# Kernel tuning notes

Measured on AMD Instinct MI355X. Metric: run time of the kernel, lower is better.

## Reference

```python
import jax, jax.numpy as jnp
import numpy as np

B, N, T, E, H, R = 8, 64, 128, 128, 8, 4
DH = E // H


def setup_inputs() -> dict:
    key = jax.random.key(0)
    ks = jax.random.split(key, 14)
    s = 1.0 / np.sqrt(E)
    return {
        "node_memory": jax.random.normal(ks[0], (B, N, T, E), jnp.float32),
        "subgraph_memory": jax.random.normal(ks[1], (B, N, T, E, R - 1), jnp.float32),
        "Wq": jax.random.normal(ks[2], (E, E), jnp.float32) * s,
        "bq": jnp.zeros((E,), jnp.float32),
        "Wk": jax.random.normal(ks[3], (E, E), jnp.float32) * s,
        "bk": jnp.zeros((E,), jnp.float32),
        "Wv": jax.random.normal(ks[4], (E, E), jnp.float32) * s,
        "bv": jnp.zeros((E,), jnp.float32),
        "in_w": jax.random.normal(ks[5], (3 * E, E), jnp.float32) * s,
        "in_b": jnp.zeros((3 * E,), jnp.float32),
        "out_w": jax.random.normal(ks[6], (E, E), jnp.float32) * s,
        "out_b": jnp.zeros((E,), jnp.float32),
        "fc_w": jax.random.normal(ks[7], (E, R * E), jnp.float32) * (1.0 / np.sqrt(R * E)),
        "fc_b": jnp.zeros((E,), jnp.float32),
    }


def reference(node_memory, subgraph_memory, Wq, bq, Wk, bk, Wv, bv,
              in_w, in_b, out_w, out_b, fc_w, fc_b):
    # combined: [B,N,T,R,E] = concat(node[...,None,:], subgraph permuted)
    combined = jnp.concatenate(
        [node_memory[..., None, :], jnp.swapaxes(subgraph_memory, -1, -2)], axis=-2)
    # outer QKV projections
    Q = jnp.einsum("bntrf,ef->bntre", combined, Wq) + bq
    K = jnp.einsum("bntrf,ef->bntre", combined, Wk) + bk
    V = jnp.einsum("bntrf,ef->bntre", combined, Wv) + bv
    # nn.MultiheadAttention in-projection
    q = jnp.einsum("bntre,fe->bntrf", Q, in_w[:E]) + in_b[:E]
    k = jnp.einsum("bntre,fe->bntrf", K, in_w[E:2 * E]) + in_b[E:2 * E]
    v = jnp.einsum("bntre,fe->bntrf", V, in_w[2 * E:]) + in_b[2 * E:]
    # split heads: [B,N,T,R,H,DH]
    q = q.reshape(B, N, T, R, H, DH) * (1.0 / np.sqrt(DH))
    k = k.reshape(B, N, T, R, H, DH)
    v = v.reshape(B, N, T, R, H, DH)
    scores = jnp.einsum("bntrhd,bntshd->bnthrs", q, k)  # [B,N,T,H,R,R]
    attn = jax.nn.softmax(scores, axis=-1)
    o = jnp.einsum("bnthrs,bntshd->bntrhd", attn, v).reshape(B, N, T, R, E)
    o = jnp.einsum("bntre,fe->bntrf", o, out_w) + out_b
    # concat the R representations and fuse
    o = o.reshape(B, N, T, R * E)
    return jnp.einsum("bntc,ec->bnte", o, fc_w) + fc_b
```

## Files before the change

kernel.cpp:

```cpp
#include <hip/hip_runtime.h>
#include <hip/hip_bf16.h>

constexpr int cE  = 128;
constexpr int cR  = 4;
constexpr int cNT = 65536;

typedef short s8v  __attribute__((ext_vector_type(8)));
typedef float f4v  __attribute__((ext_vector_type(4)));

static __device__ __forceinline__ unsigned short f2bf(float x) {
    union { float f; unsigned int u; } v; v.f = x;
    unsigned int r = v.u + 0x7fffu + ((v.u >> 16) & 1u);
    return (unsigned short)(r >> 16);
}

#define QB(x, C) __int_as_float(__builtin_amdgcn_update_dpp( \
            0, __float_as_int(x), C, 0xF, 0xF, false))

__global__ __launch_bounds__(256) void k_prep(
    const float* __restrict__ Wq, const float* __restrict__ Wk, const float* __restrict__ Wv,
    const float* __restrict__ in_w, const float* __restrict__ out_w, const float* __restrict__ fc_w,
    const float* __restrict__ bq, const float* __restrict__ bk, const float* __restrict__ bv,
    const float* __restrict__ in_b, const float* __restrict__ out_b, const float* __restrict__ fc_b,
    unsigned short* __restrict__ wqkv, unsigned short* __restrict__ meff,
    float* __restrict__ bqkv, float* __restrict__ beff)
{
    int bid = blockIdx.x;
    if (bid < 1792) {
        int gt = bid * 256 + (int)threadIdx.x;
        int o  = gt >> 2;
        int p  = gt & 3;
        float s;
        if (o < 3 * cE * cE) {
            int w   = o >> 14;
            int rem = o & (cE * cE - 1);
            int f = rem >> 7, g = rem & 127;
            const float* Wsel = (w == 0) ? Wq : ((w == 1) ? Wk : Wv);
            const float* iw = in_w + (size_t)(w * cE + f) * cE + p * 32;
            const float* wp = Wsel + (size_t)(p * 32) * cE + g;
            float s0 = 0.f, s1 = 0.f;
            #pragma unroll
            for (int e = 0; e < 32; e += 2) {
                s0 += iw[e]     * wp[(size_t)e * cE];
                s1 += iw[e + 1] * wp[(size_t)(e + 1) * cE];
            }
            s = s0 + s1;
            s += __shfl_xor(s, 1);
            s += __shfl_xor(s, 2);
            if (w == 0) s *= 0.25f;
            if (p == 0) wqkv[o] = f2bf(s);
        } else {
            int i2 = o - 3 * cE * cE;
            int e1 = i2 >> 9;
            int c  = i2 & 511;
            const float* fw = fc_w + (size_t)e1 * 512 + (c >> 7) * cE + p * 32;
            int ee = c & 127;
            const float* ow = out_w + (size_t)(p * 32) * cE + ee;
            float s0 = 0.f, s1 = 0.f;
            #pragma unroll
            for (int ff = 0; ff < 32; ff += 2) {
                s0 += fw[ff]     * ow[(size_t)ff * cE];
                s1 += fw[ff + 1] * ow[(size_t)(ff + 1) * cE];
            }
            s = s0 + s1;
            s += __shfl_xor(s, 1);
            s += __shfl_xor(s, 2);
            if (p == 0) meff[i2] = f2bf(s);
        }
    } else {
        int idx = (bid - 1792) * 256 + (int)threadIdx.x;
        if (idx < 384) {
            int w = idx >> 7, f = idx & 127;
            const float* bsel = (w == 0) ? bq : ((w == 1) ? bk : bv);
            const float* iw = in_w + (size_t)(w * cE + f) * cE;
            float s = 0.f;
            for (int e = 0; e < cE; ++e) s += iw[e] * bsel[e];
            s += in_b[w * cE + f];
            if (w == 0) s *= 0.25f;
            bqkv[idx] = s;
        } else {
            int f = idx - 384;
            float s = 0.f;
            for (int c = 0; c < 512; ++c) s += fc_w[(size_t)f * 512 + c] * out_b[c & 127];
            beff[f] = s + fc_b[f];
        }
    }
}

#define TOKB   64
#define TOKC   16
#define PITCH  136
#define OPITCH 520

__global__ __launch_bounds__(512) void k_main(
    const float* __restrict__ node, const float* __restrict__ sub,
    const unsigned short* __restrict__ wqkv,
    const unsigned short* __restrict__ meff,
    const float* __restrict__ bqkv,
    const float* __restrict__ beff,
    float* __restrict__ out)
{
    __shared__ unsigned short sA[64 * PITCH];
    __shared__ unsigned short sO[16 * OPITCH];

    const int tid  = threadIdx.x;
    const int lane = tid & 63;
    const int wv   = tid >> 6;
    const int l15  = lane & 15;
    const int lq   = lane >> 4;

    const int tokBlock = blockIdx.x * TOKB;
    const int stok = tid >> 5;
    const int seg  = tid & 31;
    const int e0   = seg * 4;

    #pragma clang loop unroll(disable)
    for (int chunk = 0; chunk < TOKB / TOKC; ++chunk) {
        const int tokBase = tokBlock + chunk * TOKC;
        __syncthreads();

        {
            const float* np = node + (size_t)(tokBase + stok) * cE + e0;
            const float* sp = sub  + (size_t)(tokBase + stok) * 384 + seg * 12;
            float4 vn = *(const float4*)np;
            float4 f0 = *(const float4*)(sp + 0);
            float4 f1 = *(const float4*)(sp + 4);
            float4 f2 = *(const float4*)(sp + 8);
            *(ushort4*)&sA[(stok * cR) * PITCH + e0] =
                make_ushort4(f2bf(vn.x), f2bf(vn.y), f2bf(vn.z), f2bf(vn.w));
            *(ushort4*)&sA[(stok * cR + 1) * PITCH + e0] =
                make_ushort4(f2bf(f0.x), f2bf(f0.w), f2bf(f1.z), f2bf(f2.y));
            *(ushort4*)&sA[(stok * cR + 2) * PITCH + e0] =
                make_ushort4(f2bf(f0.y), f2bf(f1.x), f2bf(f1.w), f2bf(f2.z));
            *(ushort4*)&sA[(stok * cR + 3) * PITCH + e0] =
                make_ushort4(f2bf(f0.z), f2bf(f1.y), f2bf(f2.x), f2bf(f2.w));
        }
        __syncthreads();

        f4v qa[4], ka[4], va[4];
        #pragma unroll
        for (int rt = 0; rt < 4; ++rt) {
            qa[rt] = (f4v){0.f, 0.f, 0.f, 0.f};
            ka[rt] = (f4v){0.f, 0.f, 0.f, 0.f};
            va[rt] = (f4v){0.f, 0.f, 0.f, 0.f};
        }
        #pragma unroll
        for (int kc = 0; kc < 4; ++kc) {
            const int koff = kc * 32 + lq * 8;
            s8v a0 = *(const s8v*)&sA[(0 * 16 + l15) * PITCH + koff];
            s8v a1 = *(const s8v*)&sA[(1 * 16 + l15) * PITCH + koff];
            s8v a2 = *(const s8v*)&sA[(2 * 16 + l15) * PITCH + koff];
            s8v a3 = *(const s8v*)&sA[(3 * 16 + l15) * PITCH + koff];
            const size_t fo = (size_t)(wv * 16 + l15) * cE + koff;
            s8v wq_ = *(const s8v*)(wqkv + fo);
            s8v wk_ = *(const s8v*)(wqkv + 16384 + fo);
            s8v wv_ = *(const s8v*)(wqkv + 32768 + fo);
            qa[0] = __builtin_amdgcn_mfma_f32_16x16x32_bf16(wq_, a0, qa[0], 0, 0, 0);
            qa[1] = __builtin_amdgcn_mfma_f32_16x16x32_bf16(wq_, a1, qa[1], 0, 0, 0);
            qa[2] = __builtin_amdgcn_mfma_f32_16x16x32_bf16(wq_, a2, qa[2], 0, 0, 0);
            qa[3] = __builtin_amdgcn_mfma_f32_16x16x32_bf16(wq_, a3, qa[3], 0, 0, 0);
            ka[0] = __builtin_amdgcn_mfma_f32_16x16x32_bf16(wk_, a0, ka[0], 0, 0, 0);
            ka[1] = __builtin_amdgcn_mfma_f32_16x16x32_bf16(wk_, a1, ka[1], 0, 0, 0);
            ka[2] = __builtin_amdgcn_mfma_f32_16x16x32_bf16(wk_, a2, ka[2], 0, 0, 0);
            ka[3] = __builtin_amdgcn_mfma_f32_16x16x32_bf16(wk_, a3, ka[3], 0, 0, 0);
            va[0] = __builtin_amdgcn_mfma_f32_16x16x32_bf16(wv_, a0, va[0], 0, 0, 0);
            va[1] = __builtin_amdgcn_mfma_f32_16x16x32_bf16(wv_, a1, va[1], 0, 0, 0);
            va[2] = __builtin_amdgcn_mfma_f32_16x16x32_bf16(wv_, a2, va[2], 0, 0, 0);
            va[3] = __builtin_amdgcn_mfma_f32_16x16x32_bf16(wv_, a3, va[3], 0, 0, 0);
        }
        {
            const int fb = wv * 16 + lq * 4;
            float4 b0 = *(const float4*)(bqkv + fb);
            float4 b1 = *(const float4*)(bqkv + cE + fb);
            float4 b2 = *(const float4*)(bqkv + 2 * cE + fb);
            #pragma unroll
            for (int rt = 0; rt < 4; ++rt) {
                qa[rt][0] += b0.x; qa[rt][1] += b0.y;
                qa[rt][2] += b0.z; qa[rt][3] += b0.w;
                ka[rt][0] += b1.x; ka[rt][1] += b1.y;
                ka[rt][2] += b1.z; ka[rt][3] += b1.w;
                va[rt][0] += b2.x; va[rt][1] += b2.y;
                va[rt][2] += b2.z; va[rt][3] += b2.w;
            }
        }

        {
            const int r  = l15 & 3;
            const int tq = l15 >> 2;
            #pragma unroll
            for (int rt = 0; rt < 4; ++rt) {
                f4v q = qa[rt], k = ka[rt], v = va[rt];
                float s0 = QB(k[0],0x00)*q[0] + QB(k[1],0x00)*q[1]
                         + QB(k[2],0x00)*q[2] + QB(k[3],0x00)*q[3];
                float s1 = QB(k[0],0x55)*q[0] + QB(k[1],0x55)*q[1]
                         + QB(k[2],0x55)*q[2] + QB(k[3],0x55)*q[3];
                float s2 = QB(k[0],0xAA)*q[0] + QB(k[1],0xAA)*q[1]
                         + QB(k[2],0xAA)*q[2] + QB(k[3],0xAA)*q[3];
                float s3 = QB(k[0],0xFF)*q[0] + QB(k[1],0xFF)*q[1]
                         + QB(k[2],0xFF)*q[2] + QB(k[3],0xFF)*q[3];
                s0 += __shfl_xor(s0, 16); s0 += __shfl_xor(s0, 32);
                s1 += __shfl_xor(s1, 16); s1 += __shfl_xor(s1, 32);
                s2 += __shfl_xor(s2, 16); s2 += __shfl_xor(s2, 32);
                s3 += __shfl_xor(s3, 16); s3 += __shfl_xor(s3, 32);
                float m = fmaxf(fmaxf(s0, s1), fmaxf(s2, s3));
                float p0 = __expf(s0 - m), p1 = __expf(s1 - m);
                float p2 = __expf(s2 - m), p3 = __expf(s3 - m);
                float inv = 1.f / (p0 + p1 + p2 + p3);
                p0 *= inv; p1 *= inv; p2 *= inv; p3 *= inv;
                float o0 = p0*QB(v[0],0x00) + p1*QB(v[0],0x55)
                         + p2*QB(v[0],0xAA) + p3*QB(v[0],0xFF);
                float o1 = p0*QB(v[1],0x00) + p1*QB(v[1],0x55)
                         + p2*QB(v[1],0xAA) + p3*QB(v[1],0xFF);
                float o2 = p0*QB(v[2],0x00) + p1*QB(v[2],0x55)
                         + p2*QB(v[2],0xAA) + p3*QB(v[2],0xFF);
                float o3 = p0*QB(v[3],0x00) + p1*QB(v[3],0x55)
                         + p2*QB(v[3],0xAA) + p3*QB(v[3],0xFF);
                int tok = rt * 4 + tq;
                *(ushort4*)&sO[tok * OPITCH + r * cE + wv * 16 + lq * 4] =
                    make_ushort4(f2bf(o0), f2bf(o1), f2bf(o2), f2bf(o3));
            }
        }
        __syncthreads();

        {
            f4v acc = (f4v){0.f, 0.f, 0.f, 0.f};
            #pragma unroll 4
            for (int kc = 0; kc < 16; ++kc) {
                int koff = kc * 32 + lq * 8;
                s8v a = *(const s8v*)&sO[l15 * OPITCH + koff];
                s8v b = *(const s8v*)(meff + (size_t)(wv * 16 + l15) * 512 + koff);
                acc = __builtin_amdgcn_mfma_f32_16x16x32_bf16(b, a, acc, 0, 0, 0);
            }
            const int col = wv * 16 + lq * 4;
            float4 b4 = *(const float4*)&beff[col];
            *(float4*)&out[(size_t)(tokBase + l15) * cE + col] =
                make_float4(acc[0] + b4.x, acc[1] + b4.y,
                            acc[2] + b4.z, acc[3] + b4.w);
        }
    }
}

extern "C" void kernel_launch(void* const* d_in, const int* in_sizes, int n_in,
                              void* d_out, int out_size, void* d_ws, size_t ws_size,
                              hipStream_t stream) {
    const float* node  = (const float*)d_in[0];
    const float* sub   = (const float*)d_in[1];
    const float* Wq    = (const float*)d_in[2];
    const float* bq    = (const float*)d_in[3];
    const float* Wk    = (const float*)d_in[4];
    const float* bk    = (const float*)d_in[5];
    const float* Wv    = (const float*)d_in[6];
    const float* bv    = (const float*)d_in[7];
    const float* in_w  = (const float*)d_in[8];
    const float* in_b  = (const float*)d_in[9];
    const float* out_w = (const float*)d_in[10];
    const float* out_b = (const float*)d_in[11];
    const float* fc_w  = (const float*)d_in[12];
    const float* fc_b  = (const float*)d_in[13];

    unsigned short* ws_wqkv = (unsigned short*)d_ws;
    unsigned short* ws_meff = ws_wqkv + 3 * cE * cE;
    float* ws_bqkv = (float*)((char*)d_ws + (size_t)(3 * cE * cE + cE * cR * cE) * 2);
    float* ws_beff = ws_bqkv + 3 * cE;

    k_prep<<<dim3(1794), dim3(256), 0, stream>>>(Wq, Wk, Wv, in_w, out_w, fc_w,
                                                 bq, bk, bv, in_b, out_b, fc_b,
                                                 ws_wqkv, ws_meff, ws_bqkv, ws_beff);
    k_main<<<dim3(cNT / TOKB), dim3(512), 0, stream>>>(node, sub, ws_wqkv, ws_meff,
                                                       ws_bqkv, ws_beff, (float*)d_out);
}
```

Baseline: 327.5 us.

## Split fused attention kernel into attention stage and separate output GEMM

Splits the fused per-chunk kernel into two kernels. The first computes QKV projections and the small attention per 16-token block, writing a bf16 concatenated output to workspace. The second runs the fused out/fc projection as a tiled GEMM over 64-token blocks with LDS staging. This aims to raise parallelism and improve reuse in the final GEMM, at the cost of an extra global round-trip of the intermediate. The old fused kernel is kept as a fallback when the workspace is too small.

```diff
diff --git a/kernel.cpp b/kernel.cpp
--- a/kernel.cpp
+++ b/kernel.cpp
@@ -87,12 +87,198 @@
     }
 }
 
-#define TOKB   64
 #define TOKC   16
 #define PITCH  136
 #define OPITCH 520
 
-__global__ __launch_bounds__(512) void k_main(
+__global__ __launch_bounds__(512) void k_mainA(
+    const float* __restrict__ node, const float* __restrict__ sub,
+    const unsigned short* __restrict__ wqkv,
+    const float* __restrict__ bqkv,
+    unsigned short* __restrict__ oconcat)
+{
+    __shared__ unsigned short sA[64 * PITCH];
+
+    const int tid  = threadIdx.x;
+    const int lane = tid & 63;
+    const int wv   = tid >> 6;
+    const int l15  = lane & 15;
+    const int lq   = lane >> 4;
+
+    const int tokBase = blockIdx.x * TOKC;
+    const int stok = tid >> 5;
+    const int seg  = tid & 31;
+    const int e0   = seg * 4;
+
+    {
+        const float* np = node + (size_t)(tokBase + stok) * cE + e0;
+        const float* sp = sub  + (size_t)(tokBase + stok) * 384 + seg * 12;
+        float4 vn = *(const float4*)np;
+        float4 f0 = *(const float4*)(sp + 0);
+        float4 f1 = *(const float4*)(sp + 4);
+        float4 f2 = *(const float4*)(sp + 8);
+        *(ushort4*)&sA[(stok * cR) * PITCH + e0] =
+            make_ushort4(f2bf(vn.x), f2bf(vn.y), f2bf(vn.z), f2bf(vn.w));
+        *(ushort4*)&sA[(stok * cR + 1) * PITCH + e0] =
+            make_ushort4(f2bf(f0.x), f2bf(f0.w), f2bf(f1.z), f2bf(f2.y));
+        *(ushort4*)&sA[(stok * cR + 2) * PITCH + e0] =
+            make_ushort4(f2bf(f0.y), f2bf(f1.x), f2bf(f1.w), f2bf(f2.z));
+        *(ushort4*)&sA[(stok * cR + 3) * PITCH + e0] =
+            make_ushort4(f2bf(f0.z), f2bf(f1.y), f2bf(f2.x), f2bf(f2.w));
+    }
+    __syncthreads();
+
+    f4v qa[4], ka[4], va[4];
+    #pragma unroll
+    for (int rt = 0; rt < 4; ++rt) {
+        qa[rt] = (f4v){0.f, 0.f, 0.f, 0.f};
+        ka[rt] = (f4v){0.f, 0.f, 0.f, 0.f};
+        va[rt] = (f4v){0.f, 0.f, 0.f, 0.f};
+    }
+    #pragma unroll
+    for (int kc = 0; kc < 4; ++kc) {
+        const int koff = kc * 32 + lq * 8;
+        s8v a0 = *(const s8v*)&sA[(0 * 16 + l15) * PITCH + koff];
+        s8v a1 = *(const s8v*)&sA[(1 * 16 + l15) * PITCH + koff];
+        s8v a2 = *(const s8v*)&sA[(2 * 16 + l15) * PITCH + koff];
+        s8v a3 = *(const s8v*)&sA[(3 * 16 + l15) * PITCH + koff];
+        const size_t fo = (size_t)(wv * 16 + l15) * cE + koff;
+        s8v wq_ = *(const s8v*)(wqkv + fo);
+        s8v wk_ = *(const s8v*)(wqkv + 16384 + fo);
+        s8v wv_ = *(const s8v*)(wqkv + 32768 + fo);
+        qa[0] = __builtin_amdgcn_mfma_f32_16x16x32_bf16(wq_, a0, qa[0], 0, 0, 0);
+        qa[1] = __builtin_amdgcn_mfma_f32_16x16x32_bf16(wq_, a1, qa[1], 0, 0, 0);
+        qa[2] = __builtin_amdgcn_mfma_f32_16x16x32_bf16(wq_, a2, qa[2], 0, 0, 0);
+        qa[3] = __builtin_amdgcn_mfma_f32_16x16x32_bf16(wq_, a3, qa[3], 0, 0, 0);
+        ka[0] = __builtin_amdgcn_mfma_f32_16x16x32_bf16(wk_, a0, ka[0], 0, 0, 0);
+        ka[1] = __builtin_amdgcn_mfma_f32_16x16x32_bf16(wk_, a1, ka[1], 0, 0, 0);
+        ka[2] = __builtin_amdgcn_mfma_f32_16x16x32_bf16(wk_, a2, ka[2], 0, 0, 0);
+        ka[3] = __builtin_amdgcn_mfma_f32_16x16x32_bf16(wk_, a3, ka[3], 0, 0, 0);
+        va[0] = __builtin_amdgcn_mfma_f32_16x16x32_bf16(wv_, a0, va[0], 0, 0, 0);
+        va[1] = __builtin_amdgcn_mfma_f32_16x16x32_bf16(wv_, a1, va[1], 0, 0, 0);
+        va[2] = __builtin_amdgcn_mfma_f32_16x16x32_bf16(wv_, a2, va[2], 0, 0, 0);
+        va[3] = __builtin_amdgcn_mfma_f32_16x16x32_bf16(wv_, a3, va[3], 0, 0, 0);
+    }
+    {
+        const int fb = wv * 16 + lq * 4;
+        float4 b0 = *(const float4*)(bqkv + fb);
+        float4 b1 = *(const float4*)(bqkv + cE + fb);
+        float4 b2 = *(const float4*)(bqkv + 2 * cE + fb);
+        #pragma unroll
+        for (int rt = 0; rt < 4; ++rt) {
+            qa[rt][0] += b0.x; qa[rt][1] += b0.y;
+            qa[rt][2] += b0.z; qa[rt][3] += b0.w;
+            ka[rt][0] += b1.x; ka[rt][1] += b1.y;
+            ka[rt][2] += b1.z; ka[rt][3] += b1.w;
+            va[rt][0] += b2.x; va[rt][1] += b2.y;
+            va[rt][2] += b2.z; va[rt][3] += b2.w;
+        }
+    }
+
+    {
+        const int r  = l15 & 3;
+        const int tq = l15 >> 2;
+        #pragma unroll
+        for (int rt = 0; rt < 4; ++rt) {
+            f4v q = qa[rt], k = ka[rt], v = va[rt];
+            float s0 = QB(k[0],0x00)*q[0] + QB(k[1],0x00)*q[1]
+                     + QB(k[2],0x00)*q[2] + QB(k[3],0x00)*q[3];
+            float s1 = QB(k[0],0x55)*q[0] + QB(k[1],0x55)*q[1]
+                     + QB(k[2],0x55)*q[2] + QB(k[3],0x55)*q[3];
+            float s2 = QB(k[0],0xAA)*q[0] + QB(k[1],0xAA)*q[1]
+                     + QB(k[2],0xAA)*q[2] + QB(k[3],0xAA)*q[3];
+            float s3 = QB(k[0],0xFF)*q[0] + QB(k[1],0xFF)*q[1]
+                     + QB(k[2],0xFF)*q[2] + QB(k[3],0xFF)*q[3];
+            s0 += __shfl_xor(s0, 16); s0 += __shfl_xor(s0, 32);
+            s1 += __shfl_xor(s1, 16); s1 += __shfl_xor(s1, 32);
+            s2 += __shfl_xor(s2, 16); s2 += __shfl_xor(s2, 32);
+            s3 += __shfl_xor(s3, 16); s3 += __shfl_xor(s3, 32);
+            float m = fmaxf(fmaxf(s0, s1), fmaxf(s2, s3));
+            float p0 = __expf(s0 - m), p1 = __expf(s1 - m);
+            float p2 = __expf(s2 - m), p3 = __expf(s3 - m);
+            float inv = 1.f / (p0 + p1 + p2 + p3);
+            p0 *= inv; p1 *= inv; p2 *= inv; p3 *= inv;
+            float o0 = p0*QB(v[0],0x00) + p1*QB(v[0],0x55)
+                     + p2*QB(v[0],0xAA) + p3*QB(v[0],0xFF);
+            float o1 = p0*QB(v[1],0x00) + p1*QB(v[1],0x55)
+                     + p2*QB(v[1],0xAA) + p3*QB(v[1],0xFF);
+            float o2 = p0*QB(v[2],0x00) + p1*QB(v[2],0x55)
+                     + p2*QB(v[2],0xAA) + p3*QB(v[2],0xFF);
+            float o3 = p0*QB(v[3],0x00) + p1*QB(v[3],0x55)
+                     + p2*QB(v[3],0xAA) + p3*QB(v[3],0xFF);
+            const int tok = tokBase + rt * 4 + tq;
+            unsigned int u0 = (unsigned int)f2bf(o0) | ((unsigned int)f2bf(o1) << 16);
+            unsigned int u1 = (unsigned int)f2bf(o2) | ((unsigned int)f2bf(o3) << 16);
+            *(uint2*)&oconcat[(size_t)tok * 512 + r * cE + wv * 16 + lq * 4] =
+                make_uint2(u0, u1);
+        }
+    }
+}
+
+#define BPAD 72
+
+__global__ __launch_bounds__(256) void k_gemmB(
+    const unsigned short* __restrict__ oconcat,
+    const unsigned short* __restrict__ meff,
+    const float* __restrict__ beff,
+    float* __restrict__ out)
+{
+    __shared__ unsigned short sT[64 * BPAD];
+
+    const int tid  = threadIdx.x;
+    const int lane = tid & 63;
+    const int w    = tid >> 6;
+    const int l15  = lane & 15;
+    const int lq   = lane >> 4;
+
+    const int tokBase = blockIdx.x * 64;
+
+    f4v acc[4][2];
+    #pragma unroll
+    for (int rt = 0; rt < 4; ++rt) {
+        acc[rt][0] = (f4v){0.f, 0.f, 0.f, 0.f};
+        acc[rt][1] = (f4v){0.f, 0.f, 0.f, 0.f};
+    }
+
+    #pragma clang loop unroll(disable)
+    for (int ks = 0; ks < 8; ++ks) {
+        __syncthreads();
+        #pragma unroll
+        for (int it = 0; it < 2; ++it) {
+            const int row = it * 32 + (tid >> 3);
+            const int ko  = (tid & 7) * 8;
+            *(uint4*)&sT[row * BPAD + ko] =
+                *(const uint4*)&oconcat[(size_t)(tokBase + row) * 512 + ks * 64 + ko];
+        }
+        __syncthreads();
+        #pragma unroll
+        for (int kh = 0; kh < 2; ++kh) {
+            const int ko = kh * 32 + lq * 8;
+            s8v b0 = *(const s8v*)(meff + (size_t)(w * 32 + l15)      * 512 + ks * 64 + ko);
+            s8v b1 = *(const s8v*)(meff + (size_t)(w * 32 + 16 + l15) * 512 + ks * 64 + ko);
+            #pragma unroll
+            for (int rt = 0; rt < 4; ++rt) {
+                s8v a = *(const s8v*)&sT[(rt * 16 + l15) * BPAD + ko];
+                acc[rt][0] = __builtin_amdgcn_mfma_f32_16x16x32_bf16(b0, a, acc[rt][0], 0, 0, 0);
+                acc[rt][1] = __builtin_amdgcn_mfma_f32_16x16x32_bf16(b1, a, acc[rt][1], 0, 0, 0);
+            }
+        }
+    }
+    #pragma unroll
+    for (int cc = 0; cc < 2; ++cc) {
+        const int col = w * 32 + cc * 16 + lq * 4;
+        float4 b4 = *(const float4*)&beff[col];
+        #pragma unroll
+        for (int rt = 0; rt < 4; ++rt) {
+            *(float4*)&out[(size_t)(tokBase + rt * 16 + l15) * cE + col] =
+                make_float4(acc[rt][cc][0] + b4.x, acc[rt][cc][1] + b4.y,
+                            acc[rt][cc][2] + b4.z, acc[rt][cc][3] + b4.w);
+        }
+    }
+}
+
+#define TOKBF  64
+__global__ __launch_bounds__(512) void k_mainR11(
     const float* __restrict__ node, const float* __restrict__ sub,
     const unsigned short* __restrict__ wqkv,
     const unsigned short* __restrict__ meff,
@@ -109,16 +295,15 @@
     const int l15  = lane & 15;
     const int lq   = lane >> 4;
 
-    const int tokBlock = blockIdx.x * TOKB;
+    const int tokBlock = blockIdx.x * TOKBF;
     const int stok = tid >> 5;
     const int seg  = tid & 31;
     const int e0   = seg * 4;
 
     #pragma clang loop unroll(disable)
-    for (int chunk = 0; chunk < TOKB / TOKC; ++chunk) {
+    for (int chunk = 0; chunk < TOKBF / TOKC; ++chunk) {
         const int tokBase = tokBlock + chunk * TOKC;
         __syncthreads();
-
         {
             const float* np = node + (size_t)(tokBase + stok) * cE + e0;
             const float* sp = sub  + (size_t)(tokBase + stok) * 384 + seg * 12;
@@ -183,7 +368,6 @@
                 va[rt][2] += b2.z; va[rt][3] += b2.w;
             }
         }
-
         {
             const int r  = l15 & 3;
             const int tq = l15 >> 2;
@@ -221,7 +405,6 @@
             }
         }
         __syncthreads();
-
         {
             f4v acc = (f4v){0.f, 0.f, 0.f, 0.f};
             #pragma unroll 4
@@ -266,6 +449,17 @@
     k_prep<<<dim3(1794), dim3(256), 0, stream>>>(Wq, Wk, Wv, in_w, out_w, fc_w,
                                                  bq, bk, bv, in_b, out_b, fc_b,
                                                  ws_wqkv, ws_meff, ws_bqkv, ws_beff);
-    k_main<<<dim3(cNT / TOKB), dim3(512), 0, stream>>>(node, sub, ws_wqkv, ws_meff,
-                                                       ws_bqkv, ws_beff, (float*)d_out);
-}
+
+    const size_t oofs = (size_t)1 << 20;
+    const size_t need = oofs + (size_t)cNT * 512 * 2;
+    if (ws_size >= need) {
+        unsigned short* oconcat = (unsigned short*)((char*)d_ws + oofs);
+        k_mainA<<<dim3(cNT / TOKC), dim3(512), 0, stream>>>(
+            node, sub, ws_wqkv, ws_bqkv, oconcat);
+        k_gemmB<<<dim3(cNT / 64), dim3(256), 0, stream>>>(
+            oconcat, ws_meff, ws_beff, (float*)d_out);
+    } else {
+        k_mainR11<<<dim3(cNT / TOKBF), dim3(512), 0, stream>>>(
+            node, sub, ws_wqkv, ws_meff, ws_bqkv, ws_beff, (float*)d_out);
+    }
+}
```

Result: faster. 302.4 us (-7.7%).
